# Performance work log

Measured on AMD Instinct MI355X. Metric: run time of the kernel, lower is better.

The kernel has to match this reference:

```python
import jax, jax.numpy as jnp
import numpy as np
from math import sqrt

NUM_HEADS = 8
HIDDEN = 768
ATTN_DIM = HIDDEN // NUM_HEADS  # 96
NEG = -1e10


def setup_inputs() -> dict:
    key = jax.random.key(0)
    ks = jax.random.split(key, 6)
    b, s, dim = 8, 1024, 768
    scale = 1.0 / sqrt(dim)
    return {
        "span_embeddings": jax.random.normal(ks[0], (b, s, dim), dtype=jnp.float32),
        "span_tags": jax.random.randint(ks[1], (b, s), 0, 5),
        "w_weight": jax.random.normal(ks[2], (1, dim), dtype=jnp.float32) * scale,
        "w_q": jax.random.normal(ks[3], (HIDDEN, dim), dtype=jnp.float32) * scale,
        "w_k": jax.random.normal(ks[4], (HIDDEN, dim), dtype=jnp.float32) * scale,
        "w_v": jax.random.normal(ks[5], (HIDDEN, dim), dtype=jnp.float32) * scale,
    }


def reference(span_embeddings, span_tags, w_weight, w_q, w_k, w_v):
    b, s, _ = span_embeddings.shape
    pad = span_tags == 0  # [b, s]

    # additive span attention weights: Linear(dim -> 1), mask padded, softmax over seq
    attn_weights = span_embeddings @ w_weight.T  # [b, s, 1]
    attn_weights = jnp.where(pad[:, :, None], NEG, attn_weights)
    attn_weights = jax.nn.softmax(attn_weights, axis=1)

    # NOTE: original views hidden as (attn_dim, num_heads) in that order
    qs = (span_embeddings @ w_q.T).reshape(b, s, ATTN_DIM, NUM_HEADS)
    ks = (span_embeddings @ w_k.T).reshape(b, s, ATTN_DIM, NUM_HEADS)
    vs = (span_embeddings @ w_v.T).reshape(b, s, ATTN_DIM, NUM_HEADS)

    rel = jnp.einsum('bqdh,bkdh->bqkh', qs, ks) / sqrt(ATTN_DIM)  # [b,q,k,h]
    # original masks along query axis (relevance_weights[span_tags.eq(0)] = NEG)
    rel = jnp.where(pad[:, :, None, None], NEG, rel)
    # original softmax(dim=-1) -> over the HEADS axis (faithful quirk)
    rel = jax.nn.softmax(rel, axis=-1)

    span_value = jnp.einsum('bqkh,bkdh->bqdh', rel, vs).reshape(b, s, HIDDEN)
    weighted_value = jnp.sum(attn_weights * span_value, axis=1)  # [b, hidden]
    return weighted_value
```

## Files before the change

kernel.cpp:

```cpp
#include <hip/hip_runtime.h>
#include <hip/hip_bf16.h>
#include <math.h>

#define NEGV (-1e10f)

typedef __attribute__((ext_vector_type(8))) short bf16x8;
typedef __attribute__((ext_vector_type(4))) float f32x4;

static __device__ __forceinline__ unsigned short f2bf(float f) {
  unsigned int u = __builtin_bit_cast(unsigned int, f);
  unsigned int r = (u + 0x7fffu + ((u >> 16) & 1u)) >> 16;
  return (unsigned short)r;
}
static __device__ __forceinline__ float bf2f(unsigned short v) {
  return __builtin_bit_cast(float, (unsigned int)v << 16);
}

#define GLD16(g, l)                                                   \
  __builtin_amdgcn_global_load_lds(                                   \
      (const __attribute__((address_space(1))) void*)(g),             \
      (__attribute__((address_space(3))) void*)(l), 16, 0, 0)

__global__ __launch_bounds__(256) void cast_emb_logits(
    const float* __restrict__ emb, const int* __restrict__ tags,
    const float* __restrict__ ww, unsigned short* __restrict__ embbf,
    float* __restrict__ logits) {
  int w = threadIdx.x >> 6, lane = threadIdx.x & 63;
  int row = blockIdx.x * 4 + w;
  const float4* src = (const float4*)(emb + (size_t)row * 768);
  const float4* wsrc = (const float4*)ww;
  ushort4* dst = (ushort4*)(embbf + (size_t)row * 768);
  float d = 0.f;
#pragma unroll
  for (int j = 0; j < 3; j++) {
    int idx = lane + 64 * j;
    float4 v = src[idx];
    float4 wv = wsrc[idx];
    d += v.x * wv.x + v.y * wv.y + v.z * wv.z + v.w * wv.w;
    ushort4 o;
    o.x = f2bf(v.x); o.y = f2bf(v.y); o.z = f2bf(v.z); o.w = f2bf(v.w);
    dst[idx] = o;
  }
#pragma unroll
  for (int off = 32; off; off >>= 1) d += __shfl_xor(d, off);
  if (lane == 0) logits[row] = (tags[row] == 0) ? NEGV : d;
}

__global__ __launch_bounds__(256) void cast_w(
    const float* __restrict__ wq, const float* __restrict__ wk,
    const float* __restrict__ wv, unsigned short* __restrict__ out) {
  int z = blockIdx.y;
  const float* src = (z == 0) ? wq : (z == 1) ? wk : wv;
  int idx = blockIdx.x * 256 + threadIdx.x;
  float4 v = ((const float4*)src)[idx];
  ushort4 o;
  o.x = f2bf(v.x); o.y = f2bf(v.y); o.z = f2bf(v.z); o.w = f2bf(v.w);
  ((ushort4*)(out + (size_t)z * 589824))[idx] = o;
}

__global__ __launch_bounds__(256) void softmax_aw(
    const float* __restrict__ logits, float* __restrict__ aw) {
  __shared__ float red[4];
  int b = blockIdx.x, t = threadIdx.x;
  const float* L = logits + b * 1024;
  float x0 = L[t], x1 = L[t + 256], x2 = L[t + 512], x3 = L[t + 768];
  float m = fmaxf(fmaxf(x0, x1), fmaxf(x2, x3));
#pragma unroll
  for (int off = 32; off; off >>= 1) m = fmaxf(m, __shfl_xor(m, off));
  if ((t & 63) == 0) red[t >> 6] = m;
  __syncthreads();
  m = fmaxf(fmaxf(red[0], red[1]), fmaxf(red[2], red[3]));
  float e0 = __expf(x0 - m), e1 = __expf(x1 - m), e2 = __expf(x2 - m),
        e3 = __expf(x3 - m);
  float s = e0 + e1 + e2 + e3;
#pragma unroll
  for (int off = 32; off; off >>= 1) s += __shfl_xor(s, off);
  __syncthreads();
  if ((t & 63) == 0) red[t >> 6] = s;
  __syncthreads();
  float inv = 1.0f / (red[0] + red[1] + red[2] + red[3]);
  float* A = aw + b * 1024;
  A[t] = e0 * inv; A[t + 256] = e1 * inv;
  A[t + 512] = e2 * inv; A[t + 768] = e3 * inv;
}

__global__ __launch_bounds__(256) void qkv_gemm(
    const unsigned short* __restrict__ A, const unsigned short* __restrict__ Wbf,
    unsigned short* __restrict__ Qf, unsigned short* __restrict__ Kf,
    unsigned short* __restrict__ Vbf) {
  __shared__ __align__(16) unsigned short sm[16896];
  unsigned short* As = sm;
  unsigned short* Bs = sm + 8192;
  int z = blockIdx.z;
  const unsigned short* B = Wbf + (size_t)z * 589824;
  int mb = blockIdx.x * 128, nb = blockIdx.y * 128;
  int tid = threadIdx.x;
  int w = tid >> 6, lane = tid & 63;
  int wm = w >> 1, wn = w & 1;
  int c = lane & 15, quad = lane >> 4;
  int lrow = lane >> 2, lcol = (lane & 3) * 8;
  const unsigned short* Ag = A + (size_t)(mb + w * 32 + lrow) * 768 + lcol;
  const unsigned short* Bg = B + (size_t)(nb + w * 32 + lrow) * 768 + lcol;
  int woff = w * 1024;

#define PREFETCH(buf, kb)                                              \
  do {                                                                 \
    GLD16(Ag + (kb), As + (buf) * 4096 + woff);                        \
    GLD16(Ag + (kb) + 16 * 768, As + (buf) * 4096 + woff + 512);       \
    GLD16(Bg + (kb), Bs + (buf) * 4096 + woff);                        \
    GLD16(Bg + (kb) + 16 * 768, Bs + (buf) * 4096 + woff + 512);       \
  } while (0)

  f32x4 acc[4][4];
#pragma unroll
  for (int i = 0; i < 4; i++)
#pragma unroll
    for (int j = 0; j < 4; j++) acc[i][j] = 0;

  PREFETCH(0, 0);
  for (int it = 0; it < 24; it++) {
    __syncthreads();
    if (it + 1 < 24) PREFETCH((it + 1) & 1, (it + 1) * 32);
    const unsigned short* Ab = As + (it & 1) * 4096;
    const unsigned short* Bb = Bs + (it & 1) * 4096;
    bf16x8 af[4], bfr[4];
#pragma unroll
    for (int i = 0; i < 4; i++)
      af[i] = *(const bf16x8*)&Ab[(wm * 64 + i * 16 + c) * 32 + quad * 8];
#pragma unroll
    for (int j = 0; j < 4; j++)
      bfr[j] = *(const bf16x8*)&Bb[(wn * 64 + j * 16 + c) * 32 + quad * 8];
#pragma unroll
    for (int i = 0; i < 4; i++)
#pragma unroll
      for (int j = 0; j < 4; j++)
        acc[i][j] = __builtin_amdgcn_mfma_f32_16x16x32_bf16(af[i], bfr[j],
                                                            acc[i][j], 0, 0, 0);
  }
  __syncthreads();

  if (z == 2) {
#pragma unroll
    for (int i = 0; i < 4; i++)
#pragma unroll
      for (int j = 0; j < 4; j++)
#pragma unroll
        for (int r = 0; r < 4; r++) {
          int rowg = mb + wm * 64 + i * 16 + quad * 4 + r;
          int colg = nb + wn * 64 + j * 16 + c;
          Vbf[(size_t)rowg * 768 + colg] = f2bf(acc[i][j][r]);
        }
  } else {
    unsigned short* O = (z == 0) ? Qf : Kf;
#pragma unroll
    for (int i = 0; i < 4; i++) {
      int qt = wm * 4 + i;
#pragma unroll
      for (int j = 0; j < 4; j++) {
#pragma unroll
        for (int r = 0; r < 4; r++) {
          int run = qt * 8 + (c & 7);
          int l32 = (quad * 4 + r) | (wn << 4);
          int e = j * 2 + (c >> 3);
          sm[run * 264 + l32 * 8 + e] = f2bf(acc[i][j][r]);
        }
      }
    }
    __syncthreads();
    int bq = mb >> 10;
    int qtg0 = (mb & 1023) >> 4;
    int tt = blockIdx.y >> 1;
    int halfoff = (blockIdx.y & 1) * 256;
#pragma unroll
    for (int it2 = 0; it2 < 8; it2++) {
      int g = it2 * 256 + tid;
      int run = g >> 5, l32 = g & 31;
      int qt = run >> 3, h = run & 7;
      bf16x8 vdat = *(const bf16x8*)&sm[run * 264 + l32 * 8];
      size_t dst =
          (((size_t)(bq * 64 + qtg0 + qt) * 8 + h) * 3 + tt) * 512 +
          halfoff + l32 * 8;
      *(bf16x8*)&O[dst] = vdat;
    }
  }
#undef PREFETCH
}

__global__ __launch_bounds__(256) void attn(
    const unsigned short* __restrict__ Qf, const unsigned short* __restrict__ Kf,
    const float* __restrict__ aw, float* __restrict__ Ptp) {
  int b = blockIdx.z;
  int qc = blockIdx.y;
  int kt = blockIdx.x * 4 + (threadIdx.x >> 6);
  int lane = threadIdx.x & 63;
  int quad = lane >> 4;
  const unsigned short* Kb =
      Kf + (size_t)(b * 64 + kt) * 12288 + (size_t)lane * 8;
  bf16x8 kfr[8][3];
#pragma unroll
  for (int h = 0; h < 8; h++)
#pragma unroll
    for (int t = 0; t < 3; t++)
      kfr[h][t] = *(const bf16x8*)(Kb + (h * 3 + t) * 512);
  float partial[8];
#pragma unroll
  for (int h = 0; h < 8; h++) partial[h] = 0.f;
  const float scale = 0.10206207261596577f;
  for (int qi = 0; qi < 4; qi++) {
    int qt = qc * 4 + qi;
    const unsigned short* Qb =
        Qf + (size_t)(b * 64 + qt) * 12288 + (size_t)lane * 8;
    f32x4 s[8];
#pragma unroll
    for (int h = 0; h < 8; h++) {
      f32x4 sh = 0;
#pragma unroll
      for (int t = 0; t < 3; t++) {
        bf16x8 qfr = *(const bf16x8*)(Qb + (h * 3 + t) * 512);
        sh = __builtin_amdgcn_mfma_f32_16x16x32_bf16(qfr, kfr[h][t], sh, 0, 0, 0);
      }
      s[h] = sh;
    }
    f32x4 al = *(const f32x4*)(aw + b * 1024 + qt * 16 + quad * 4);
#pragma unroll
    for (int r = 0; r < 4; r++) {
      float v[8], m = -1e30f;
#pragma unroll
      for (int h = 0; h < 8; h++) {
        v[h] = s[h][r] * scale;
        m = fmaxf(m, v[h]);
      }
      float ssum = 0.f;
#pragma unroll
      for (int h = 0; h < 8; h++) {
        float e = __expf(v[h] - m);
        v[h] = e;
        ssum += e;
      }
      float g = al[r] * __builtin_amdgcn_rcpf(ssum);
#pragma unroll
      for (int h = 0; h < 8; h++) partial[h] += v[h] * g;
    }
  }
#pragma unroll
  for (int h = 0; h < 8; h++) {
    float v = partial[h];
    v += __shfl_xor(v, 16);
    v += __shfl_xor(v, 32);
    partial[h] = v;
  }
  if (lane < 16) {
#pragma unroll
    for (int h = 0; h < 8; h++)
      Ptp[(((size_t)qc * 8 + b) * 1024 + kt * 16 + lane) * 8 + h] = partial[h];
  }
}

__global__ __launch_bounds__(256) void finalize(
    const float* __restrict__ Ptp, const unsigned short* __restrict__ Vbf,
    float* __restrict__ out) {
  __shared__ float ps[1024];
  int kc = blockIdx.x, b = blockIdx.y;
  int t = threadIdx.x;
#pragma unroll
  for (int j = 0; j < 4; j++) {
    int idx = t + j * 256;
    int k = kc * 128 + (idx >> 3), h = idx & 7;
    float s = 0.f;
#pragma unroll
    for (int qc = 0; qc < 16; qc++)
      s += Ptp[(((size_t)qc * 8 + b) * 1024 + k) * 8 + h];
    ps[idx] = s;
  }
  __syncthreads();
  int h = t & 7;
  float a0 = 0, a1 = 0, a2 = 0;
  const unsigned short* Vb = Vbf + ((size_t)b * 1024 + kc * 128) * 768;
  for (int kk = 0; kk < 128; kk++) {
    float p = ps[kk * 8 + h];
    const unsigned short* vr = Vb + (size_t)kk * 768;
    a0 += p * bf2f(vr[t]);
    a1 += p * bf2f(vr[t + 256]);
    a2 += p * bf2f(vr[t + 512]);
  }
  atomicAdd(&out[b * 768 + t], a0);
  atomicAdd(&out[b * 768 + t + 256], a1);
  atomicAdd(&out[b * 768 + t + 512], a2);
}

extern "C" void kernel_launch(void* const* d_in, const int* in_sizes, int n_in,
                              void* d_out, int out_size, void* d_ws,
                              size_t ws_size, hipStream_t stream) {
  const float* emb = (const float*)d_in[0];
  const int* tags = (const int*)d_in[1];
  const float* ww = (const float*)d_in[2];
  const float* wq = (const float*)d_in[3];
  const float* wk = (const float*)d_in[4];
  const float* wv = (const float*)d_in[5];
  float* out = (float*)d_out;
  char* ws = (char*)d_ws;
  unsigned short* embbf = (unsigned short*)(ws + 0);
  unsigned short* wbf   = (unsigned short*)(ws + 12582912);
  unsigned short* Qf    = (unsigned short*)(ws + 16121856);
  unsigned short* Kf    = (unsigned short*)(ws + 28704768);
  unsigned short* Vbf   = (unsigned short*)(ws + 41287680);
  float* logits         = (float*)(ws + 53870592);
  float* aw             = (float*)(ws + 53903360);
  float* Ptp            = (float*)(ws + 53936128);

  hipMemsetAsync(out, 0, 8 * 768 * sizeof(float), stream);
  cast_emb_logits<<<2048, 256, 0, stream>>>(emb, tags, ww, embbf, logits);
  cast_w<<<dim3(576, 3), 256, 0, stream>>>(wq, wk, wv, wbf);
  softmax_aw<<<8, 256, 0, stream>>>(logits, aw);
  qkv_gemm<<<dim3(64, 6, 3), 256, 0, stream>>>(embbf, wbf, Qf, Kf, Vbf);
  attn<<<dim3(16, 16, 8), 256, 0, stream>>>(Qf, Kf, aw, Ptp);
  finalize<<<dim3(8, 8), 256, 0, stream>>>(Ptp, Vbf, out);
}
```

Baseline: 186.4 us.

## Retile attention to 32x32 MFMA with LDS-staged double-buffered Q/K per head

The QKV GEMM epilogue now writes Q and K in a 32-row fragment layout matching the 32x32x16 bf16 MFMA. The attention kernel computes a 64x64 query-key tile per block, staging Q and K for each head through double-buffered LDS via global_load_lds, so each K fragment is reused across more queries. Previously each wave held K in registers and reloaded Q from global memory. The per-head softmax uses exp2 with a prescaled constant, and partials are reduced across waves in LDS before writing. Finalize gets four times as many blocks, each covering 32 keys, to raise parallelism, at the cost of more atomics.

```diff
diff --git a/kernel.cpp b/kernel.cpp
--- a/kernel.cpp
+++ b/kernel.cpp
@@ -6,6 +6,7 @@
 
 typedef __attribute__((ext_vector_type(8))) short bf16x8;
 typedef __attribute__((ext_vector_type(4))) float f32x4;
+typedef __attribute__((ext_vector_type(16))) float f32x16;
 
 static __device__ __forceinline__ unsigned short f2bf(float f) {
   unsigned int u = __builtin_bit_cast(unsigned int, f);
@@ -88,7 +89,7 @@
     const unsigned short* __restrict__ A, const unsigned short* __restrict__ Wbf,
     unsigned short* __restrict__ Qf, unsigned short* __restrict__ Kf,
     unsigned short* __restrict__ Vbf) {
-  __shared__ __align__(16) unsigned short sm[16896];
+  __shared__ __align__(16) unsigned short sm[16640];
   unsigned short* As = sm;
   unsigned short* Bs = sm + 8192;
   int z = blockIdx.z;
@@ -154,32 +155,31 @@
     unsigned short* O = (z == 0) ? Qf : Kf;
 #pragma unroll
     for (int i = 0; i < 4; i++) {
-      int qt = wm * 4 + i;
 #pragma unroll
       for (int j = 0; j < 4; j++) {
 #pragma unroll
         for (int r = 0; r < 4; r++) {
-          int run = qt * 8 + (c & 7);
-          int l32 = (quad * 4 + r) | (wn << 4);
-          int e = j * 2 + (c >> 3);
-          sm[run * 264 + l32 * 8 + e] = f2bf(acc[i][j][r]);
+          int ql = wm * 64 + i * 16 + quad * 4 + r;
+          int h = c & 7;
+          int elem = j * 2 + (c >> 3);
+          int chunkL = (ql >> 5) * 8 + h;
+          int lane32 = (ql & 31) + wn * 32;
+          sm[chunkL * 520 + lane32 * 8 + elem] = f2bf(acc[i][j][r]);
         }
       }
     }
     __syncthreads();
     int bq = mb >> 10;
-    int qtg0 = (mb & 1023) >> 4;
-    int tt = blockIdx.y >> 1;
-    int halfoff = (blockIdx.y & 1) * 256;
+    int qt32g0 = (mb & 1023) >> 5;
+    int tt = blockIdx.y;
 #pragma unroll
     for (int it2 = 0; it2 < 8; it2++) {
       int g = it2 * 256 + tid;
-      int run = g >> 5, l32 = g & 31;
-      int qt = run >> 3, h = run & 7;
-      bf16x8 vdat = *(const bf16x8*)&sm[run * 264 + l32 * 8];
-      size_t dst =
-          (((size_t)(bq * 64 + qtg0 + qt) * 8 + h) * 3 + tt) * 512 +
-          halfoff + l32 * 8;
+      int chunkL = g >> 6;
+      int off = (g & 63) * 8;
+      bf16x8 vdat = *(const bf16x8*)&sm[chunkL * 520 + off];
+      int qt32 = qt32g0 + (chunkL >> 3), h = chunkL & 7;
+      size_t dst = ((((size_t)(bq * 32 + qt32) * 8 + h) * 6 + tt) << 9) + off;
       *(bf16x8*)&O[dst] = vdat;
     }
   }
@@ -189,94 +189,116 @@
 __global__ __launch_bounds__(256) void attn(
     const unsigned short* __restrict__ Qf, const unsigned short* __restrict__ Kf,
     const float* __restrict__ aw, float* __restrict__ Ptp) {
-  int b = blockIdx.z;
-  int qc = blockIdx.y;
-  int kt = blockIdx.x * 4 + (threadIdx.x >> 6);
-  int lane = threadIdx.x & 63;
-  int quad = lane >> 4;
-  const unsigned short* Kb =
-      Kf + (size_t)(b * 64 + kt) * 12288 + (size_t)lane * 8;
-  bf16x8 kfr[8][3];
-#pragma unroll
-  for (int h = 0; h < 8; h++)
-#pragma unroll
-    for (int t = 0; t < 3; t++)
-      kfr[h][t] = *(const bf16x8*)(Kb + (h * 3 + t) * 512);
+  __shared__ __align__(16) unsigned short Qs[2 * 6144];
+  __shared__ __align__(16) unsigned short Ks[2 * 6144];
+  __shared__ float pbuf[1024];
+  int b = blockIdx.z, qb = blockIdx.y, kb = blockIdx.x;
+  int tid = threadIdx.x, w = tid >> 6, lane = tid & 63;
+  int wq = w >> 1, wk = w & 1;
+
+#define STAGE(hh, buf)                                                        \
+  do {                                                                        \
+    _Pragma("unroll") for (int call = 0; call < 3; call++) {                  \
+      int cc = call * 4 + w;                                                  \
+      int qt32 = (cc >= 6) ? 1 : 0;                                           \
+      int t5 = cc - qt32 * 6;                                                 \
+      size_t go = ((((size_t)(b * 32 + qb * 2 + qt32) * 8 + (hh)) * 6 + t5)   \
+                   << 9) + lane * 8;                                          \
+      size_t ko = ((((size_t)(b * 32 + kb * 2 + qt32) * 8 + (hh)) * 6 + t5)   \
+                   << 9) + lane * 8;                                          \
+      GLD16(Qf + go, Qs + (buf) * 6144 + cc * 512);                           \
+      GLD16(Kf + ko, Ks + (buf) * 6144 + cc * 512);                           \
+    }                                                                         \
+  } while (0)
+
+  f32x16 acc[8];
+#pragma unroll
+  for (int h = 0; h < 8; h++) acc[h] = 0;
+
+  STAGE(0, 0);
+#pragma unroll
+  for (int h = 0; h < 8; h++) {
+    __syncthreads();
+    if (h + 1 < 8) STAGE(h + 1, (h + 1) & 1);
+    const unsigned short* Qb = Qs + (h & 1) * 6144;
+    const unsigned short* Kb = Ks + (h & 1) * 6144;
+#pragma unroll
+    for (int t = 0; t < 6; t++) {
+      bf16x8 a = *(const bf16x8*)&Qb[(wq * 6 + t) * 512 + lane * 8];
+      bf16x8 bb = *(const bf16x8*)&Kb[(wk * 6 + t) * 512 + lane * 8];
+      acc[h] = __builtin_amdgcn_mfma_f32_32x32x16_bf16(a, bb, acc[h], 0, 0, 0);
+    }
+  }
+
+  float awv[16];
+#pragma unroll
+  for (int reg = 0; reg < 16; reg++) {
+    int row = (reg & 3) + 8 * (reg >> 2) + 4 * (lane >> 5);
+    awv[reg] = aw[b * 1024 + qb * 64 + wq * 32 + row];
+  }
   float partial[8];
 #pragma unroll
   for (int h = 0; h < 8; h++) partial[h] = 0.f;
-  const float scale = 0.10206207261596577f;
-  for (int qi = 0; qi < 4; qi++) {
-    int qt = qc * 4 + qi;
-    const unsigned short* Qb =
-        Qf + (size_t)(b * 64 + qt) * 12288 + (size_t)lane * 8;
-    f32x4 s[8];
+  const float C2 = 0.10206207261596577f * 1.4426950408889634f;
+#pragma unroll
+  for (int reg = 0; reg < 16; reg++) {
+    float v[8], m = -1e30f;
 #pragma unroll
     for (int h = 0; h < 8; h++) {
-      f32x4 sh = 0;
-#pragma unroll
-      for (int t = 0; t < 3; t++) {
-        bf16x8 qfr = *(const bf16x8*)(Qb + (h * 3 + t) * 512);
-        sh = __builtin_amdgcn_mfma_f32_16x16x32_bf16(qfr, kfr[h][t], sh, 0, 0, 0);
-      }
-      s[h] = sh;
-    }
-    f32x4 al = *(const f32x4*)(aw + b * 1024 + qt * 16 + quad * 4);
-#pragma unroll
-    for (int r = 0; r < 4; r++) {
-      float v[8], m = -1e30f;
-#pragma unroll
-      for (int h = 0; h < 8; h++) {
-        v[h] = s[h][r] * scale;
-        m = fmaxf(m, v[h]);
-      }
-      float ssum = 0.f;
-#pragma unroll
-      for (int h = 0; h < 8; h++) {
-        float e = __expf(v[h] - m);
-        v[h] = e;
-        ssum += e;
-      }
-      float g = al[r] * __builtin_amdgcn_rcpf(ssum);
-#pragma unroll
-      for (int h = 0; h < 8; h++) partial[h] += v[h] * g;
-    }
+      v[h] = acc[h][reg] * C2;
+      m = fmaxf(m, v[h]);
+    }
+    float ssum = 0.f;
+#pragma unroll
+    for (int h = 0; h < 8; h++) {
+      float e = exp2f(v[h] - m);
+      v[h] = e;
+      ssum += e;
+    }
+    float g = awv[reg] * __builtin_amdgcn_rcpf(ssum);
+#pragma unroll
+    for (int h = 0; h < 8; h++) partial[h] += v[h] * g;
   }
 #pragma unroll
   for (int h = 0; h < 8; h++) {
     float v = partial[h];
-    v += __shfl_xor(v, 16);
     v += __shfl_xor(v, 32);
     partial[h] = v;
   }
-  if (lane < 16) {
-#pragma unroll
-    for (int h = 0; h < 8; h++)
-      Ptp[(((size_t)qc * 8 + b) * 1024 + kt * 16 + lane) * 8 + h] = partial[h];
-  }
+  if (lane < 32) {
+#pragma unroll
+    for (int h = 0; h < 8; h++) pbuf[w * 256 + lane * 8 + h] = partial[h];
+  }
+  __syncthreads();
+#pragma unroll
+  for (int wk2 = 0; wk2 < 2; wk2++) {
+    float s = pbuf[wk2 * 256 + tid] + pbuf[(2 + wk2) * 256 + tid];
+    int kcol = tid >> 3, h = tid & 7;
+    Ptp[(((size_t)qb * 8 + b) * 1024 + kb * 64 + wk2 * 32 + kcol) * 8 + h] = s;
+  }
+#undef STAGE
 }
 
 __global__ __launch_bounds__(256) void finalize(
     const float* __restrict__ Ptp, const unsigned short* __restrict__ Vbf,
     float* __restrict__ out) {
-  __shared__ float ps[1024];
+  __shared__ float ps[256];
   int kc = blockIdx.x, b = blockIdx.y;
   int t = threadIdx.x;
-#pragma unroll
-  for (int j = 0; j < 4; j++) {
-    int idx = t + j * 256;
-    int k = kc * 128 + (idx >> 3), h = idx & 7;
+  {
+    int k = kc * 32 + (t >> 3), h = t & 7;
     float s = 0.f;
 #pragma unroll
     for (int qc = 0; qc < 16; qc++)
       s += Ptp[(((size_t)qc * 8 + b) * 1024 + k) * 8 + h];
-    ps[idx] = s;
+    ps[t] = s;
   }
   __syncthreads();
   int h = t & 7;
   float a0 = 0, a1 = 0, a2 = 0;
-  const unsigned short* Vb = Vbf + ((size_t)b * 1024 + kc * 128) * 768;
-  for (int kk = 0; kk < 128; kk++) {
+  const unsigned short* Vb = Vbf + ((size_t)b * 1024 + kc * 32) * 768;
+#pragma unroll 4
+  for (int kk = 0; kk < 32; kk++) {
     float p = ps[kk * 8 + h];
     const unsigned short* vr = Vb + (size_t)kk * 768;
     a0 += p * bf2f(vr[t]);
@@ -314,5 +336,5 @@
   softmax_aw<<<8, 256, 0, stream>>>(logits, aw);
   qkv_gemm<<<dim3(64, 6, 3), 256, 0, stream>>>(embbf, wbf, Qf, Kf, Vbf);
   attn<<<dim3(16, 16, 8), 256, 0, stream>>>(Qf, Kf, aw, Ptp);
-  finalize<<<dim3(8, 8), 256, 0, stream>>>(Ptp, Vbf, out);
-}
+  finalize<<<dim3(32, 8), 256, 0, stream>>>(Ptp, Vbf, out);
+}
```

Result: no change. 188.1 us (+1.0%).
